# Kernel optimization log

Measured on AMD Instinct MI355X. Metric: run time of the kernel, lower is better.

The kernel has to match this reference:

```python
import jax, jax.numpy as jnp
from jax import lax
import numpy as np

B, T, I, H, C = 32, 256, 128, 128, 100


def setup_inputs() -> dict:
    key = jax.random.key(0)
    ks = jax.random.split(key, 9)
    s = 1.0 / np.sqrt(H)  # PyTorch LSTMCell init range
    inp = {
        "x": jax.random.normal(ks[0], (B, T, I), dtype=jnp.float32),
        "w_ih": jax.random.uniform(ks[1], (4 * H, I), jnp.float32, -s, s),
        "b_ih": jax.random.uniform(ks[2], (4 * H,), jnp.float32, -s, s),
        "w_hh": jax.random.uniform(ks[3], (4 * H, H), jnp.float32, -s, s),
        "b_hh": jax.random.uniform(ks[4], (4 * H,), jnp.float32, -s, s),
        # attention params: normal(mean=0, std=0.01) per the source
        "w1": 0.01 * jax.random.normal(ks[5], (2 * H, H), dtype=jnp.float32),
        "w2": 0.01 * jax.random.normal(ks[6], (H, 1), dtype=jnp.float32),
        "w_fc": jax.random.uniform(ks[7], (C, H), jnp.float32, -s, s),
        "b_fc": jax.random.uniform(ks[8], (C,), jnp.float32, -s, s),
    }
    return inp


def _forward(x, w_ih, b_ih, w_hh, b_hh, w1, w2, w_fc, b_fc):
    Bv, Tv, _ = x.shape
    Hv = w_hh.shape[1]
    h0 = jnp.zeros((Bv, Hv), x.dtype)
    c0 = jnp.zeros((Bv, Hv), x.dtype)
    # memory buffer: slot 0 holds the initial zero hidden state (as in the
    # torch code, h_old starts as h_t=0); slots 1..T filled as we go.
    # Unwritten (future) slots are zero, so their attn contribution
    # attn_w * h_old is exactly zero -> no mask needed, matching the
    # growing-memory semantics of the original loop.
    mem0 = jnp.zeros((Bv, Tv + 1, Hv), x.dtype)
    attn0 = jnp.zeros((Bv, Hv), x.dtype)

    def step(carry, inp):
        h, c, mem, _ = carry
        x_t, i = inp
        # PyTorch LSTMCell: gate order i, f, g, o
        gates = x_t @ w_ih.T + b_ih + h @ w_hh.T + b_hh
        ig, fg, gg, og = jnp.split(gates, 4, axis=-1)
        c = jax.nn.sigmoid(fg) * c + jax.nn.sigmoid(ig) * jnp.tanh(gg)
        h = jax.nn.sigmoid(og) * jnp.tanh(c)
        # additive attention scores over the memory (NO softmax in source)
        h_rep = jnp.broadcast_to(h[:, None, :], mem.shape)  # [B, T+1, H]
        cat = jnp.concatenate([h_rep, mem], axis=-1)        # [B, T+1, 2H]
        s = jnp.tanh(cat @ w1) @ w2                          # [B, T+1, 1]
        attn_c = jnp.sum(s * mem, axis=1)                    # [B, H]
        mem = mem.at[:, i + 1, :].set(h)  # append h_t to memory
        return (h, c, mem, attn_c), None

    xs = (jnp.transpose(x, (1, 0, 2)), jnp.arange(Tv))
    (h, c, mem, attn_c), _ = lax.scan(step, (h0, c0, mem0, attn0), xs)
    return (h + attn_c) @ w_fc.T + b_fc


def reference(x, w_ih, b_ih, w_hh, b_hh, w1, w2, w_fc, b_fc):
    return _forward(x, w_ih, b_ih, w_hh, b_hh, w1, w2, w_fc, b_fc)
```

## Files before the change

kernel.cpp:

```cpp
#include <hip/hip_runtime.h>
#include <hip/hip_bf16.h>


#define Bsz 32
#define Tsz 256
#define Isz 128
#define Hsz 128
#define Csz 100
#define G4H 512

typedef short v8s __attribute__((ext_vector_type(8)));
typedef float v4fa __attribute__((ext_vector_type(4)));

__device__ __forceinline__ float2 pk_fma(float2 a, float2 b, float2 c) {
    float2 d;
    asm("v_pk_fma_f32 %0, %1, %2, %3" : "=v"(d) : "v"(a), "v"(b), "v"(c));
    return d;
}
__device__ __forceinline__ float quad_rsum(float x) {
    int t = __builtin_amdgcn_update_dpp(0, __float_as_int(x), 0xB1, 0xF, 0xF, true);
    x += __int_as_float(t);
    t = __builtin_amdgcn_update_dpp(0, __float_as_int(x), 0x4E, 0xF, 0xF, true);
    x += __int_as_float(t);
    return x;
}
__device__ __forceinline__ float rcpf(float x) { return __builtin_amdgcn_rcpf(x); }
__device__ __forceinline__ float ex2(float x) { return __builtin_amdgcn_exp2f(x); }
__device__ __forceinline__ float sigm_n(float x) {
    return rcpf(1.0f + ex2(-1.442695041f * x));
}
__device__ __forceinline__ float tanh_n(float x) {
    return fmaf(-2.0f, rcpf(1.0f + ex2(2.885390082f * x)), 1.0f);
}
__device__ __forceinline__ short bf16_bits(float x) {
    __hip_bfloat16 h = __float2bfloat16(x);
    return *reinterpret_cast<short*>(&h);
}
__device__ __forceinline__ float bf16_val(float x) {
    return __bfloat162float(__float2bfloat16(x));
}

__global__ __launch_bounds__(256) void prep_kernel(
    const float* __restrict__ w_ih, const float* __restrict__ b_ih,
    const float* __restrict__ w_hh, const float* __restrict__ b_hh,
    const float* __restrict__ w1,
    __hip_bfloat16* __restrict__ W2ih, __hip_bfloat16* __restrict__ W2v,
    float* __restrict__ whh_pk, float* __restrict__ bias,
    float* __restrict__ attn_c) {
    int idx = blockIdx.x * blockDim.x + threadIdx.x;
    if (idx < G4H * Isz) {
        int n = idx >> 7;
        int k = idx & 127;
        float x = w_ih[idx];
        __hip_bfloat16 hi = __float2bfloat16(x);
        __hip_bfloat16 lo = __float2bfloat16(x - __bfloat162float(hi));
        W2ih[(size_t)n * 384 + k] = hi;
        W2ih[(size_t)n * 384 + 128 + k] = lo;
        W2ih[(size_t)n * 384 + 256 + k] = hi;

        int j4  = idx & 3;
        int q   = (idx >> 2) & 3;
        int d   = (idx >> 4) & 127;
        int gi  = (idx >> 11) & 3;
        int kk4 = (idx >> 13) & 7;
        whh_pk[idx] = w_hh[(size_t)((gi << 7) + d) * 128 + (q << 5) + (kk4 << 2) + j4];
    }
    if (idx < Hsz * Hsz) {
        int n = idx >> 7;
        int k = idx & 127;
        float x = w1[(size_t)(128 + k) * Hsz + n];
        __hip_bfloat16 hi = __float2bfloat16(x);
        __hip_bfloat16 lo = __float2bfloat16(x - __bfloat162float(hi));
        W2v[(size_t)n * 384 + k] = hi;
        W2v[(size_t)n * 384 + 128 + k] = lo;
        W2v[(size_t)n * 384 + 256 + k] = hi;
    }
    if (idx < G4H) bias[idx] = b_ih[idx] + b_hh[idx];
    if (idx < Bsz * Hsz) attn_c[idx] = 0.0f;
}

__global__ __launch_bounds__(256) void gemm_mfma_f32a(
    const float* __restrict__ A, const __hip_bfloat16* __restrict__ W2,
    const float* __restrict__ bias, float* __restrict__ C, int M, int N) {
    const int tid = threadIdx.x;
    const int w = tid >> 6, lane = tid & 63;
    const int m0 = blockIdx.y * 64 + (w & 1) * 32;
    const int n0 = blockIdx.x * 64 + (w >> 1) * 32;
    const int r = lane & 15, quad = lane >> 4;

    v8s Ahi[2][4], Alo[2][4];
    #pragma unroll
    for (int i = 0; i < 2; ++i)
        #pragma unroll
        for (int cb = 0; cb < 4; ++cb) {
            const float* src = A + (size_t)(m0 + 16 * i + r) * Isz + cb * 32 + quad * 8;
            float4 f0 = *(const float4*)src;
            float4 f1 = *(const float4*)(src + 4);
            float f[8] = {f0.x, f0.y, f0.z, f0.w, f1.x, f1.y, f1.z, f1.w};
            v8s hi, lo;
            #pragma unroll
            for (int e = 0; e < 8; ++e) {
                float hv = bf16_val(f[e]);
                hi[e] = bf16_bits(f[e]);
                lo[e] = bf16_bits(f[e] - hv);
            }
            Ahi[i][cb] = hi;
            Alo[i][cb] = lo;
        }

    v4fa acc[2][2] = {};
    const short* Wb = (const short*)W2;
    #pragma unroll
    for (int ks = 0; ks < 12; ++ks) {
        int cb = ks & 3;
        v8s a0 = (ks >= 8) ? Alo[0][cb] : Ahi[0][cb];
        v8s a1 = (ks >= 8) ? Alo[1][cb] : Ahi[1][cb];
        int kb = ks * 32 + quad * 8;
        v8s b0 = *(const v8s*)(Wb + (size_t)(n0 + r) * 384 + kb);
        v8s b1 = *(const v8s*)(Wb + (size_t)(n0 + 16 + r) * 384 + kb);
        acc[0][0] = __builtin_amdgcn_mfma_f32_16x16x32_bf16(a0, b0, acc[0][0], 0, 0, 0);
        acc[0][1] = __builtin_amdgcn_mfma_f32_16x16x32_bf16(a0, b1, acc[0][1], 0, 0, 0);
        acc[1][0] = __builtin_amdgcn_mfma_f32_16x16x32_bf16(a1, b0, acc[1][0], 0, 0, 0);
        acc[1][1] = __builtin_amdgcn_mfma_f32_16x16x32_bf16(a1, b1, acc[1][1], 0, 0, 0);
    }
    #pragma unroll
    for (int i = 0; i < 2; ++i)
        #pragma unroll
        for (int j = 0; j < 2; ++j) {
            int cn = n0 + 16 * j + r;
            float bb = bias ? bias[cn] : 0.0f;
            #pragma unroll
            for (int rr = 0; rr < 4; ++rr) {
                int row = m0 + 16 * i + quad * 4 + rr;
                C[(size_t)row * N + cn] = acc[i][j][rr] + bb;
            }
        }
}

#define HPAD(k) ((k) + 8 * ((k) >> 5))

__global__ __launch_bounds__(512, 2) void lstm_seq(
    const float* __restrict__ G, const float* __restrict__ whh_pk,
    float* __restrict__ H_all) {
    const int b = blockIdx.x;
    const int tid = threadIdx.x;
    const int d = tid >> 2;
    const int q = tid & 3;

    __shared__ float h_s[2][160];

    float2 w2v[4][16];
    {
        const float4* wp = (const float4*)whh_pk;
        #pragma unroll
        for (int kk4 = 0; kk4 < 8; ++kk4)
            #pragma unroll
            for (int gi = 0; gi < 4; ++gi) {
                float4 v = wp[((kk4 * 4 + gi) * 128 + d) * 4 + q];
                w2v[gi][kk4 * 2]     = make_float2(v.x, v.y);
                w2v[gi][kk4 * 2 + 1] = make_float2(v.z, v.w);
            }
    }

    if (tid < 320) ((float*)h_s)[tid] = 0.0f;
    float c = 0.0f;
    __syncthreads();

    const float* Gq = G + (size_t)b * Tsz * G4H + q * 128 + d;
    float* Hst = H_all + (size_t)b * Tsz * Hsz + d;

    float gval = Gq[0];
    int cur = 0;
    for (int t = 0; t < Tsz; ++t) {
        const int tn = (t < Tsz - 1) ? t + 1 : t;
        float ngval = Gq[(size_t)tn * G4H];

        float2 accA[4], accB[4];
        #pragma unroll
        for (int gi = 0; gi < 4; ++gi) {
            accA[gi] = make_float2(q == gi ? gval : 0.f, 0.f);
            accB[gi] = make_float2(0.f, 0.f);
        }
        const float4* hb4 = (const float4*)&h_s[cur][q * 40];
        #pragma unroll
        for (int kk4 = 0; kk4 < 8; ++kk4) {
            float4 h4 = hb4[kk4];
            float2 hA = make_float2(h4.x, h4.y);
            float2 hB = make_float2(h4.z, h4.w);
            accA[0] = pk_fma(hA, w2v[0][2 * kk4], accA[0]);
            accA[1] = pk_fma(hA, w2v[1][2 * kk4], accA[1]);
            accA[2] = pk_fma(hA, w2v[2][2 * kk4], accA[2]);
            accA[3] = pk_fma(hA, w2v[3][2 * kk4], accA[3]);
            accB[0] = pk_fma(hB, w2v[0][2 * kk4 + 1], accB[0]);
            accB[1] = pk_fma(hB, w2v[1][2 * kk4 + 1], accB[1]);
            accB[2] = pk_fma(hB, w2v[2][2 * kk4 + 1], accB[2]);
            accB[3] = pk_fma(hB, w2v[3][2 * kk4 + 1], accB[3]);
        }
        float a0 = quad_rsum(accA[0].x + accA[0].y + accB[0].x + accB[0].y);
        float a1 = quad_rsum(accA[1].x + accA[1].y + accB[1].x + accB[1].y);
        float a2 = quad_rsum(accA[2].x + accA[2].y + accB[2].x + accB[2].y);
        float a3 = quad_rsum(accA[3].x + accA[3].y + accB[3].x + accB[3].y);

        float iv = sigm_n(a0);
        float fv = sigm_n(a1);
        float gv = tanh_n(a2);
        float ov = sigm_n(a3);
        c = fmaf(fv, c, iv * gv);
        float h = ov * tanh_n(c);

        if (q == 0) {
            h_s[cur ^ 1][HPAD(d)] = h;
            Hst[(size_t)t * Hsz] = h;
        }
        gval = ngval;
        __builtin_amdgcn_sched_barrier(0);
        asm volatile("s_waitcnt lgkmcnt(0)" ::: "memory");
        __builtin_amdgcn_s_barrier();
        __builtin_amdgcn_sched_barrier(0);
        cur ^= 1;
    }
}

__global__ __launch_bounds__(256) void kv_scores(
    const float* __restrict__ H_all, const __hip_bfloat16* __restrict__ W2v,
    const float* __restrict__ w1, const float* __restrict__ w2,
    float* __restrict__ attn_c) {
    const int b = blockIdx.x >> 2, jt = blockIdx.x & 3;
    const int tid = threadIdx.x;
    __shared__ float kv_s[64][132];
    __shared__ float hT[Hsz];
    __shared__ float q_s[Hsz];
    __shared__ float w2s[Hsz];
    __shared__ float s_s[64];
    __shared__ float part[2][Hsz];

    const float* Hb = H_all + (size_t)b * Tsz * Hsz;

    if (tid < Hsz) {
        hT[tid] = Hb[255 * Hsz + tid];
        w2s[tid] = w2[tid];
    }

    {
        const int w = tid >> 6, lane = tid & 63;
        const int m0 = (w & 1) * 32;
        const int n0 = (w >> 1) * 32;
        const int r = lane & 15, quad = lane >> 4;
        const float* Abase = Hb + (size_t)(jt * 64) * Hsz;

        v8s Ahi[2][4], Alo[2][4];
        #pragma unroll
        for (int i = 0; i < 2; ++i)
            #pragma unroll
            for (int cb = 0; cb < 4; ++cb) {
                const float* src = Abase + (size_t)(m0 + 16 * i + r) * Hsz + cb * 32 + quad * 8;
                float4 f0 = *(const float4*)src;
                float4 f1 = *(const float4*)(src + 4);
                float f[8] = {f0.x, f0.y, f0.z, f0.w, f1.x, f1.y, f1.z, f1.w};
                v8s hi, lo;
                #pragma unroll
                for (int e = 0; e < 8; ++e) {
                    float hv = bf16_val(f[e]);
                    hi[e] = bf16_bits(f[e]);
                    lo[e] = bf16_bits(f[e] - hv);
                }
                Ahi[i][cb] = hi;
                Alo[i][cb] = lo;
            }

        v4fa acc[2][2][2] = {};
        const short* Wb = (const short*)W2v;
        #pragma unroll
        for (int ks = 0; ks < 12; ++ks) {
            int cb = ks & 3;
            v8s a0 = (ks >= 8) ? Alo[0][cb] : Ahi[0][cb];
            v8s a1 = (ks >= 8) ? Alo[1][cb] : Ahi[1][cb];
            int kb = ks * 32 + quad * 8;
            #pragma unroll
            for (int nh = 0; nh < 2; ++nh) {
                int nn = nh * 64 + n0;
                v8s b0 = *(const v8s*)(Wb + (size_t)(nn + r) * 384 + kb);
                v8s b1 = *(const v8s*)(Wb + (size_t)(nn + 16 + r) * 384 + kb);
                acc[nh][0][0] = __builtin_amdgcn_mfma_f32_16x16x32_bf16(a0, b0, acc[nh][0][0], 0, 0, 0);
                acc[nh][0][1] = __builtin_amdgcn_mfma_f32_16x16x32_bf16(a0, b1, acc[nh][0][1], 0, 0, 0);
                acc[nh][1][0] = __builtin_amdgcn_mfma_f32_16x16x32_bf16(a1, b0, acc[nh][1][0], 0, 0, 0);
                acc[nh][1][1] = __builtin_amdgcn_mfma_f32_16x16x32_bf16(a1, b1, acc[nh][1][1], 0, 0, 0);
            }
        }
        #pragma unroll
        for (int nh = 0; nh < 2; ++nh)
            #pragma unroll
            for (int i = 0; i < 2; ++i)
                #pragma unroll
                for (int j = 0; j < 2; ++j)
                    #pragma unroll
                    for (int rr = 0; rr < 4; ++rr)
                        kv_s[m0 + 16 * i + quad * 4 + rr][nh * 64 + n0 + 16 * j + r] =
                            acc[nh][i][j][rr];
    }
    __syncthreads();

    if (tid < Hsz) {
        float acc = 0.f;
        #pragma unroll 8
        for (int k = 0; k < Hsz; ++k) acc = fmaf(hT[k], w1[k * Hsz + tid], acc);
        q_s[tid] = acc;
    }
    __syncthreads();

    const int jl = tid >> 2, ql = tid & 3;
    const int j = jt * 64 + jl;
    float p = 0.f;
    if (j < 255) {
        #pragma unroll 8
        for (int kk = 0; kk < 32; ++kk) {
            int k = ql * 32 + ((kk + ql) & 31);
            p = fmaf(tanh_n(q_s[k] + kv_s[jl][k]), w2s[k], p);
        }
    }
    p = quad_rsum(p);
    if (ql == 0) s_s[jl] = (j < 255) ? p : 0.0f;
    __syncthreads();

    {
        const int dd = tid & 127, half = tid >> 7;
        float acc = 0.f;
        #pragma unroll 4
        for (int u = 0; u < 32; ++u) {
            int lj = half * 32 + u;
            int jj = jt * 64 + lj;
            if (jj < 255) acc = fmaf(s_s[lj], Hb[(size_t)jj * Hsz + dd], acc);
        }
        part[half][dd] = acc;
    }
    __syncthreads();
    if (tid < Hsz) atomicAdd(&attn_c[b * Hsz + tid], part[0][tid] + part[1][tid]);
}

__global__ __launch_bounds__(256) void fc_out(
    const float* __restrict__ H_all, const float* __restrict__ attn_c,
    const float* __restrict__ w_fc, const float* __restrict__ b_fc,
    float* __restrict__ out) {
    const int b = blockIdx.x, tid = threadIdx.x;
    __shared__ float r_s[Hsz];
    if (tid < Hsz)
        r_s[tid] = H_all[(size_t)b * Tsz * Hsz + 255 * Hsz + tid] + attn_c[b * Hsz + tid];
    __syncthreads();
    const int o = tid >> 1, half = tid & 1;
    float acc = 0.f;
    if (o < Csz) {
        const float* wr = w_fc + (size_t)o * Hsz + half * 64;
        const float* rr = r_s + half * 64;
        #pragma unroll 8
        for (int k = 0; k < 64; ++k) acc = fmaf(rr[k], wr[k], acc);
    }
    acc += __shfl_xor(acc, 1);
    if (half == 0 && o < Csz) out[b * Csz + o] = acc + b_fc[o];
}

extern "C" void kernel_launch(void* const* d_in, const int* in_sizes, int n_in,
                              void* d_out, int out_size, void* d_ws, size_t ws_size,
                              hipStream_t stream) {
    const float* x    = (const float*)d_in[0];
    const float* w_ih = (const float*)d_in[1];
    const float* b_ih = (const float*)d_in[2];
    const float* w_hh = (const float*)d_in[3];
    const float* b_hh = (const float*)d_in[4];
    const float* w1   = (const float*)d_in[5];
    const float* w2   = (const float*)d_in[6];
    const float* w_fc = (const float*)d_in[7];
    const float* b_fc = (const float*)d_in[8];

    float* ws = (float*)d_ws;
    float* whh_pk = ws;
    float* bias   = whh_pk + 65536;
    float* attn_c = bias + 512;
    __hip_bfloat16* W2ih = (__hip_bfloat16*)(attn_c + 4096);
    __hip_bfloat16* W2v  = (__hip_bfloat16*)(attn_c + 4096 + 98304);
    float* G      = attn_c + 4096 + 98304 + 24576;
    float* H_all  = G + 4194304;

    prep_kernel<<<256, 256, 0, stream>>>(w_ih, b_ih, w_hh, b_hh, w1,
                                         W2ih, W2v, whh_pk, bias, attn_c);

    dim3 gG(G4H / 64, (Bsz * Tsz) / 64);
    gemm_mfma_f32a<<<gG, 256, 0, stream>>>(x, W2ih, bias, G, Bsz * Tsz, G4H);

    lstm_seq<<<Bsz, 512, 0, stream>>>(G, whh_pk, H_all);

    kv_scores<<<Bsz * 4, 256, 0, stream>>>(H_all, W2v, w1, w2, attn_c);

    fc_out<<<Bsz, 256, 0, stream>>>(H_all, attn_c, w_fc, b_fc, (float*)d_out);
}
```

Before: 320.5 us.

## Fuse attention scoring and FC output into the LSTM recurrence kernel

Measured after the change: 311.8 us. -2.7%, faster.

```diff
diff --git a/kernel.cpp b/kernel.cpp
--- a/kernel.cpp
+++ b/kernel.cpp
@@ -24,6 +24,15 @@
     x += __int_as_float(t);
     return x;
 }
+__device__ __forceinline__ float oct_rsum(float x) {
+    int t = __builtin_amdgcn_update_dpp(0, __float_as_int(x), 0xB1, 0xF, 0xF, true);
+    x += __int_as_float(t);
+    t = __builtin_amdgcn_update_dpp(0, __float_as_int(x), 0x4E, 0xF, 0xF, true);
+    x += __int_as_float(t);
+    t = __builtin_amdgcn_update_dpp(0, __float_as_int(x), 0x141, 0xF, 0xF, true);
+    x += __int_as_float(t);
+    return x;
+}
 __device__ __forceinline__ float rcpf(float x) { return __builtin_amdgcn_rcpf(x); }
 __device__ __forceinline__ float ex2(float x) { return __builtin_amdgcn_exp2f(x); }
 __device__ __forceinline__ float sigm_n(float x) {
@@ -45,8 +54,7 @@
     const float* __restrict__ w_hh, const float* __restrict__ b_hh,
     const float* __restrict__ w1,
     __hip_bfloat16* __restrict__ W2ih, __hip_bfloat16* __restrict__ W2v,
-    float* __restrict__ whh_pk, float* __restrict__ bias,
-    float* __restrict__ attn_c) {
+    float* __restrict__ whh_pk, float* __restrict__ bias) {
     int idx = blockIdx.x * blockDim.x + threadIdx.x;
     if (idx < G4H * Isz) {
         int n = idx >> 7;
@@ -76,7 +84,6 @@
         W2v[(size_t)n * 384 + 256 + k] = hi;
     }
     if (idx < G4H) bias[idx] = b_ih[idx] + b_hh[idx];
-    if (idx < Bsz * Hsz) attn_c[idx] = 0.0f;
 }
 
 __global__ __launch_bounds__(256) void gemm_mfma_f32a(
@@ -139,15 +146,25 @@
 
 #define HPAD(k) ((k) + 8 * ((k) >> 5))
 
-__global__ __launch_bounds__(512, 2) void lstm_seq(
+__global__ __launch_bounds__(512, 2) void lstm_fused(
     const float* __restrict__ G, const float* __restrict__ whh_pk,
-    float* __restrict__ H_all) {
+    const __hip_bfloat16* __restrict__ W2v,
+    const float* __restrict__ w1, const float* __restrict__ w2,
+    const float* __restrict__ w_fc, const float* __restrict__ b_fc,
+    float* __restrict__ H_all, float* __restrict__ out) {
     const int b = blockIdx.x;
     const int tid = threadIdx.x;
     const int d = tid >> 2;
     const int q = tid & 3;
 
     __shared__ float h_s[2][160];
+    __shared__ float kv_s[64][132];
+    __shared__ float hT_s[Hsz];
+    __shared__ float q_s[Hsz];
+    __shared__ float w2s[Hsz];
+    __shared__ float r_s[Hsz];
+    __shared__ float s_s[64];
+    __shared__ float part4[4][Hsz];
 
     float2 w2v[4][16];
     {
@@ -219,143 +236,125 @@
         __builtin_amdgcn_sched_barrier(0);
         cur ^= 1;
     }
-}
-
-__global__ __launch_bounds__(256) void kv_scores(
-    const float* __restrict__ H_all, const __hip_bfloat16* __restrict__ W2v,
-    const float* __restrict__ w1, const float* __restrict__ w2,
-    float* __restrict__ attn_c) {
-    const int b = blockIdx.x >> 2, jt = blockIdx.x & 3;
-    const int tid = threadIdx.x;
-    __shared__ float kv_s[64][132];
-    __shared__ float hT[Hsz];
-    __shared__ float q_s[Hsz];
-    __shared__ float w2s[Hsz];
-    __shared__ float s_s[64];
-    __shared__ float part[2][Hsz];
+
+    __syncthreads();
 
     const float* Hb = H_all + (size_t)b * Tsz * Hsz;
-
-    if (tid < Hsz) {
-        hT[tid] = Hb[255 * Hsz + tid];
-        w2s[tid] = w2[tid];
-    }
+    const int n_a = tid >> 2;
 
     {
-        const int w = tid >> 6, lane = tid & 63;
-        const int m0 = (w & 1) * 32;
-        const int n0 = (w >> 1) * 32;
-        const int r = lane & 15, quad = lane >> 4;
-        const float* Abase = Hb + (size_t)(jt * 64) * Hsz;
-
-        v8s Ahi[2][4], Alo[2][4];
-        #pragma unroll
-        for (int i = 0; i < 2; ++i)
-            #pragma unroll
-            for (int cb = 0; cb < 4; ++cb) {
-                const float* src = Abase + (size_t)(m0 + 16 * i + r) * Hsz + cb * 32 + quad * 8;
-                float4 f0 = *(const float4*)src;
-                float4 f1 = *(const float4*)(src + 4);
-                float f[8] = {f0.x, f0.y, f0.z, f0.w, f1.x, f1.y, f1.z, f1.w};
-                v8s hi, lo;
+        if (tid < Hsz) {
+            hT_s[tid] = h_s[cur][HPAD(tid)];
+            w2s[tid] = w2[tid];
+        }
+        float acc = 0.f;
+        #pragma unroll 8
+        for (int kk = 0; kk < 32; ++kk) {
+            int k = q * 32 + kk;
+            acc = fmaf(h_s[cur][HPAD(k)], w1[(size_t)k * Hsz + n_a], acc);
+        }
+        acc = quad_rsum(acc);
+        if (q == 0) q_s[n_a] = acc;
+    }
+    __syncthreads();
+
+    const int w_id = tid >> 6;
+    const int lane = tid & 63;
+    const int fr = lane & 15, fq = lane >> 4;
+    const int d_att = tid & 127, grp = tid >> 7;
+    float racc = 0.f;
+
+    for (int jt = 0; jt < 4; ++jt) {
+        {
+            const int m0 = (w_id & 1) * 32;
+            const int n0 = (w_id >> 1) * 32;
+            const float* Abase = Hb + (size_t)(jt * 64) * Hsz;
+
+            v8s Ahi[2][4], Alo[2][4];
+            #pragma unroll
+            for (int i = 0; i < 2; ++i)
                 #pragma unroll
-                for (int e = 0; e < 8; ++e) {
-                    float hv = bf16_val(f[e]);
-                    hi[e] = bf16_bits(f[e]);
-                    lo[e] = bf16_bits(f[e] - hv);
+                for (int cb = 0; cb < 4; ++cb) {
+                    const float* src = Abase + (size_t)(m0 + 16 * i + fr) * Hsz + cb * 32 + fq * 8;
+                    float4 f0 = *(const float4*)src;
+                    float4 f1 = *(const float4*)(src + 4);
+                    float f[8] = {f0.x, f0.y, f0.z, f0.w, f1.x, f1.y, f1.z, f1.w};
+                    v8s hi, lo;
+                    #pragma unroll
+                    for (int e = 0; e < 8; ++e) {
+                        float hv = bf16_val(f[e]);
+                        hi[e] = bf16_bits(f[e]);
+                        lo[e] = bf16_bits(f[e] - hv);
+                    }
+                    Ahi[i][cb] = hi;
+                    Alo[i][cb] = lo;
                 }
-                Ahi[i][cb] = hi;
-                Alo[i][cb] = lo;
-            }
-
-        v4fa acc[2][2][2] = {};
-        const short* Wb = (const short*)W2v;
-        #pragma unroll
-        for (int ks = 0; ks < 12; ++ks) {
-            int cb = ks & 3;
-            v8s a0 = (ks >= 8) ? Alo[0][cb] : Ahi[0][cb];
-            v8s a1 = (ks >= 8) ? Alo[1][cb] : Ahi[1][cb];
-            int kb = ks * 32 + quad * 8;
-            #pragma unroll
-            for (int nh = 0; nh < 2; ++nh) {
-                int nn = nh * 64 + n0;
-                v8s b0 = *(const v8s*)(Wb + (size_t)(nn + r) * 384 + kb);
-                v8s b1 = *(const v8s*)(Wb + (size_t)(nn + 16 + r) * 384 + kb);
-                acc[nh][0][0] = __builtin_amdgcn_mfma_f32_16x16x32_bf16(a0, b0, acc[nh][0][0], 0, 0, 0);
-                acc[nh][0][1] = __builtin_amdgcn_mfma_f32_16x16x32_bf16(a0, b1, acc[nh][0][1], 0, 0, 0);
-                acc[nh][1][0] = __builtin_amdgcn_mfma_f32_16x16x32_bf16(a1, b0, acc[nh][1][0], 0, 0, 0);
-                acc[nh][1][1] = __builtin_amdgcn_mfma_f32_16x16x32_bf16(a1, b1, acc[nh][1][1], 0, 0, 0);
-            }
-        }
-        #pragma unroll
-        for (int nh = 0; nh < 2; ++nh)
+
+            v4fa a2[2][2] = {};
+            const short* Wb = (const short*)W2v;
+            #pragma unroll
+            for (int ks = 0; ks < 12; ++ks) {
+                int cb = ks & 3;
+                v8s a0 = (ks >= 8) ? Alo[0][cb] : Ahi[0][cb];
+                v8s a1 = (ks >= 8) ? Alo[1][cb] : Ahi[1][cb];
+                int kb = ks * 32 + fq * 8;
+                v8s b0 = *(const v8s*)(Wb + (size_t)(n0 + fr) * 384 + kb);
+                v8s b1 = *(const v8s*)(Wb + (size_t)(n0 + 16 + fr) * 384 + kb);
+                a2[0][0] = __builtin_amdgcn_mfma_f32_16x16x32_bf16(a0, b0, a2[0][0], 0, 0, 0);
+                a2[0][1] = __builtin_amdgcn_mfma_f32_16x16x32_bf16(a0, b1, a2[0][1], 0, 0, 0);
+                a2[1][0] = __builtin_amdgcn_mfma_f32_16x16x32_bf16(a1, b0, a2[1][0], 0, 0, 0);
+                a2[1][1] = __builtin_amdgcn_mfma_f32_16x16x32_bf16(a1, b1, a2[1][1], 0, 0, 0);
+            }
             #pragma unroll
             for (int i = 0; i < 2; ++i)
                 #pragma unroll
                 for (int j = 0; j < 2; ++j)
                     #pragma unroll
                     for (int rr = 0; rr < 4; ++rr)
-                        kv_s[m0 + 16 * i + quad * 4 + rr][nh * 64 + n0 + 16 * j + r] =
-                            acc[nh][i][j][rr];
-    }
-    __syncthreads();
-
-    if (tid < Hsz) {
+                        kv_s[m0 + 16 * i + fq * 4 + rr][n0 + 16 * j + fr] = a2[i][j][rr];
+        }
+        __syncthreads();
+
+        {
+            const int jl = tid >> 3, oct = tid & 7;
+            float p = 0.f;
+            #pragma unroll
+            for (int kk = 0; kk < 16; ++kk) {
+                int k = oct * 16 + kk;
+                p = fmaf(tanh_n(q_s[k] + kv_s[jl][k]), w2s[k], p);
+            }
+            p = oct_rsum(p);
+            if (oct == 0) s_s[jl] = (jt * 64 + jl < 255) ? p : 0.0f;
+        }
+        __syncthreads();
+
+        #pragma unroll 4
+        for (int u = 0; u < 16; ++u) {
+            int lj = grp * 16 + u;
+            racc = fmaf(s_s[lj], Hb[(size_t)(jt * 64 + lj) * Hsz + d_att], racc);
+        }
+        __syncthreads();
+    }
+
+    part4[grp][d_att] = racc;
+    __syncthreads();
+    if (tid < Hsz)
+        r_s[tid] = hT_s[tid] + part4[0][tid] + part4[1][tid] + part4[2][tid] + part4[3][tid];
+    __syncthreads();
+
+    {
+        const int o = tid >> 2;
         float acc = 0.f;
-        #pragma unroll 8
-        for (int k = 0; k < Hsz; ++k) acc = fmaf(hT[k], w1[k * Hsz + tid], acc);
-        q_s[tid] = acc;
-    }
-    __syncthreads();
-
-    const int jl = tid >> 2, ql = tid & 3;
-    const int j = jt * 64 + jl;
-    float p = 0.f;
-    if (j < 255) {
-        #pragma unroll 8
-        for (int kk = 0; kk < 32; ++kk) {
-            int k = ql * 32 + ((kk + ql) & 31);
-            p = fmaf(tanh_n(q_s[k] + kv_s[jl][k]), w2s[k], p);
-        }
-    }
-    p = quad_rsum(p);
-    if (ql == 0) s_s[jl] = (j < 255) ? p : 0.0f;
-    __syncthreads();
-
-    {
-        const int dd = tid & 127, half = tid >> 7;
-        float acc = 0.f;
-        #pragma unroll 4
-        for (int u = 0; u < 32; ++u) {
-            int lj = half * 32 + u;
-            int jj = jt * 64 + lj;
-            if (jj < 255) acc = fmaf(s_s[lj], Hb[(size_t)jj * Hsz + dd], acc);
-        }
-        part[half][dd] = acc;
-    }
-    __syncthreads();
-    if (tid < Hsz) atomicAdd(&attn_c[b * Hsz + tid], part[0][tid] + part[1][tid]);
-}
-
-__global__ __launch_bounds__(256) void fc_out(
-    const float* __restrict__ H_all, const float* __restrict__ attn_c,
-    const float* __restrict__ w_fc, const float* __restrict__ b_fc,
-    float* __restrict__ out) {
-    const int b = blockIdx.x, tid = threadIdx.x;
-    __shared__ float r_s[Hsz];
-    if (tid < Hsz)
-        r_s[tid] = H_all[(size_t)b * Tsz * Hsz + 255 * Hsz + tid] + attn_c[b * Hsz + tid];
-    __syncthreads();
-    const int o = tid >> 1, half = tid & 1;
-    float acc = 0.f;
-    if (o < Csz) {
-        const float* wr = w_fc + (size_t)o * Hsz + half * 64;
-        const float* rr = r_s + half * 64;
-        #pragma unroll 8
-        for (int k = 0; k < 64; ++k) acc = fmaf(rr[k], wr[k], acc);
-    }
-    acc += __shfl_xor(acc, 1);
-    if (half == 0 && o < Csz) out[b * Csz + o] = acc + b_fc[o];
+        if (o < Csz) {
+            #pragma unroll 8
+            for (int kk = 0; kk < 32; ++kk) {
+                int k = q * 32 + kk;
+                acc = fmaf(r_s[k], w_fc[(size_t)o * Hsz + k], acc);
+            }
+        }
+        acc = quad_rsum(acc);
+        if (q == 0 && o < Csz) out[b * Csz + o] = acc + b_fc[o];
+    }
 }
 
 extern "C" void kernel_launch(void* const* d_in, const int* in_sizes, int n_in,
@@ -374,21 +373,17 @@
     float* ws = (float*)d_ws;
     float* whh_pk = ws;
     float* bias   = whh_pk + 65536;
-    float* attn_c = bias + 512;
-    __hip_bfloat16* W2ih = (__hip_bfloat16*)(attn_c + 4096);
-    __hip_bfloat16* W2v  = (__hip_bfloat16*)(attn_c + 4096 + 98304);
-    float* G      = attn_c + 4096 + 98304 + 24576;
+    __hip_bfloat16* W2ih = (__hip_bfloat16*)(bias + 512);
+    __hip_bfloat16* W2v  = (__hip_bfloat16*)(bias + 512 + 98304);
+    float* G      = bias + 512 + 98304 + 24576;
     float* H_all  = G + 4194304;
 
     prep_kernel<<<256, 256, 0, stream>>>(w_ih, b_ih, w_hh, b_hh, w1,
-                                         W2ih, W2v, whh_pk, bias, attn_c);
+                                         W2ih, W2v, whh_pk, bias);
 
     dim3 gG(G4H / 64, (Bsz * Tsz) / 64);
     gemm_mfma_f32a<<<gG, 256, 0, stream>>>(x, W2ih, bias, G, Bsz * Tsz, G4H);
 
-    lstm_seq<<<Bsz, 512, 0, stream>>>(G, whh_pk, H_all);
-
-    kv_scores<<<Bsz * 4, 256, 0, stream>>>(H_all, W2v, w1, w2, attn_c);
-
-    fc_out<<<Bsz, 256, 0, stream>>>(H_all, attn_c, w_fc, b_fc, (float*)d_out);
-}
+    lstm_fused<<<Bsz, 512, 0, stream>>>(G, whh_pk, W2v, w1, w2, w_fc, b_fc,
+                                        H_all, (float*)d_out);
+}
```
